# Kernel tuning notes

Measured on AMD Instinct MI355X. Metric: run time of the kernel, lower is better.

Reference implementation:

```python
import jax, jax.numpy as jnp
import numpy as np

N_NODES = 100000
N_EDGES = 1600000
IN_FEATS, N_HIDDEN, N_CLASSES = 128, 128, 32


def setup_inputs() -> dict:
    key = jax.random.key(0)
    ks = jax.random.split(key, 9)
    x = jax.random.normal(ks[0], (N_NODES, IN_FEATS), dtype=jnp.float32)
    src = jax.random.randint(ks[1], (N_EDGES,), 0, N_NODES, dtype=jnp.int64)
    dst = jax.random.randint(ks[2], (N_EDGES,), 0, N_NODES, dtype=jnp.int64)
    s1 = 1.0 / np.sqrt(IN_FEATS)
    s2 = 1.0 / np.sqrt(N_HIDDEN)
    W1 = jax.random.uniform(ks[3], (IN_FEATS, N_HIDDEN), jnp.float32, -s1, s1)
    b1 = jnp.zeros((N_HIDDEN,), jnp.float32)
    W2 = jax.random.uniform(ks[4], (N_HIDDEN, N_HIDDEN), jnp.float32, -s2, s2)
    b2 = jnp.zeros((N_HIDDEN,), jnp.float32)
    W3 = jax.random.uniform(ks[5], (N_HIDDEN, N_CLASSES), jnp.float32, -s2, s2)
    b3 = jnp.zeros((N_CLASSES,), jnp.float32)
    return {"x": x, "W1": W1, "b1": b1, "W2": W2, "b2": b2, "W3": W3, "b3": b3,
            "src": src, "dst": dst}


def _norms(src, dst):
    ones = jnp.ones((src.shape[0],), jnp.float32)
    deg_out = jax.ops.segment_sum(ones, src, num_segments=N_NODES)
    deg_in = jax.ops.segment_sum(ones, dst, num_segments=N_NODES)
    inv_sqrt = lambda d: jnp.where(d > 0, jax.lax.rsqrt(jnp.maximum(d, 1.0)), 0.0)
    return inv_sqrt(deg_out), inv_sqrt(deg_in)


def _sgconv(h, W, b, src, dst, norm_src, norm_dst):
    # D^-1/2 A D^-1/2 h, then linear
    m = h * norm_src[:, None]          # scale by source (out-degree) norm
    msg = m[src]                        # [E, F] gather
    agg = jax.ops.segment_sum(msg, dst, num_segments=N_NODES)  # scatter-add
    agg = agg * norm_dst[:, None]
    return agg @ W + b


def reference(x, W1, b1, W2, b2, W3, b3, src, dst):
    norm_src, norm_dst = _norms(src, dst)
    h = _sgconv(x, W1, b1, src, dst, norm_src, norm_dst)
    h = jax.nn.relu(h)
    h = _sgconv(h, W2, b2, src, dst, norm_src, norm_dst)
    h = jax.nn.relu(h)
    h = _sgconv(h, W3, b3, src, dst, norm_src, norm_dst)
    return h
```

## Files before the change

### kernel.cpp

```cpp
#include <hip/hip_runtime.h>


constexpr int FEAT = 128;
constexpr int STRIDE = 48;

typedef float f32x4 __attribute__((ext_vector_type(4)));
typedef short bf16x8 __attribute__((ext_vector_type(8)));

__device__ __forceinline__ unsigned short f2bf(float f) {
    unsigned int u = __builtin_bit_cast(unsigned int, f);
    unsigned int r = (u + 0x7FFFu + ((u >> 16) & 1u)) >> 16;
    return (unsigned short)r;
}
__device__ __forceinline__ float bf2f(unsigned short h) {
    unsigned int u = ((unsigned int)h) << 16;
    return __builtin_bit_cast(float, u);
}
__device__ __forceinline__ float bflo(unsigned int u) {
    return __builtin_bit_cast(float, u << 16);
}
__device__ __forceinline__ float bfhi(unsigned int u) {
    return __builtin_bit_cast(float, u & 0xffff0000u);
}
__device__ __forceinline__ unsigned int pack2(float a, float b) {
    return (unsigned int)f2bf(a) | ((unsigned int)f2bf(b) << 16);
}

__global__ __launch_bounds__(256) void degree_fill_kernel(const int* __restrict__ src,
                                                          const int* __restrict__ dst,
                                                          int* __restrict__ deg_out,
                                                          int* __restrict__ deg_in,
                                                          int* __restrict__ csr_pad, int E)
{
    int e = blockIdx.x * 256 + threadIdx.x;
    if (e < E) {
        int s = src[e];
        int d = dst[e];
        atomicAdd(&deg_out[s], 1);
        int pos = atomicAdd(&deg_in[d], 1);
        if (pos < STRIDE)
            csr_pad[(size_t)d * STRIDE + pos] = s;
    }
}

__global__ __launch_bounds__(256) void norm_kernel(const int* __restrict__ dout,
                                                   const int* __restrict__ din,
                                                   float* __restrict__ nsrc,
                                                   float* __restrict__ ndst, int N)
{
    int i = blockIdx.x * 256 + threadIdx.x;
    if (i < N) {
        int a = dout[i], b = din[i];
        nsrc[i] = (a > 0) ? rsqrtf((float)a) : 0.f;
        ndst[i] = (b > 0) ? rsqrtf((float)b) : 0.f;
    }
}

__global__ __launch_bounds__(256) void scale_bf16_kernel(const float* __restrict__ x,
                                                         const float* __restrict__ nsrc,
                                                         unsigned short* __restrict__ xb,
                                                         int ngroups)
{
    int i = blockIdx.x * 256 + threadIdx.x;
    if (i >= ngroups) return;
    int row = i >> 5;
    float ns = nsrc[row];
    float4 v = reinterpret_cast<const float4*>(x)[i];
    ushort4 o;
    o.x = f2bf(v.x * ns); o.y = f2bf(v.y * ns);
    o.z = f2bf(v.z * ns); o.w = f2bf(v.w * ns);
    reinterpret_cast<ushort4*>(xb)[i] = o;
}

__global__ __launch_bounds__(256) void gather128_kernel(const unsigned short* __restrict__ hb,
                                                        const float* __restrict__ ndst,
                                                        const int* __restrict__ deg_in,
                                                        const int* __restrict__ csr_pad,
                                                        unsigned short* __restrict__ aggb,
                                                        int N)
{
    const int node = blockIdx.x * 16 + (threadIdx.x >> 4);
    const int c = (threadIdx.x & 15) * 8;
    if (node >= N) return;
    const int* idx = csr_pad + (size_t)node * STRIDE;
    const int deg = min(deg_in[node], STRIDE);
    float4 a0 = make_float4(0.f, 0.f, 0.f, 0.f);
    float4 a1 = make_float4(0.f, 0.f, 0.f, 0.f);
    int j = 0;
    for (; j + 8 <= deg; j += 8) {
        int s[8];
        #pragma unroll
        for (int u = 0; u < 8; ++u) s[u] = idx[j + u];
        #pragma unroll
        for (int u = 0; u < 8; ++u) {
            uint4 v = *reinterpret_cast<const uint4*>(hb + (size_t)s[u] * 128 + c);
            a0.x += bflo(v.x); a0.y += bfhi(v.x);
            a0.z += bflo(v.y); a0.w += bfhi(v.y);
            a1.x += bflo(v.z); a1.y += bfhi(v.z);
            a1.z += bflo(v.w); a1.w += bfhi(v.w);
        }
    }
    for (; j < deg; ++j) {
        uint4 v = *reinterpret_cast<const uint4*>(hb + (size_t)idx[j] * 128 + c);
        a0.x += bflo(v.x); a0.y += bfhi(v.x);
        a0.z += bflo(v.y); a0.w += bfhi(v.y);
        a1.x += bflo(v.z); a1.y += bfhi(v.z);
        a1.z += bflo(v.w); a1.w += bfhi(v.w);
    }
    const float nd = ndst[node];
    uint4 o;
    o.x = pack2(a0.x * nd, a0.y * nd);
    o.y = pack2(a0.z * nd, a0.w * nd);
    o.z = pack2(a1.x * nd, a1.y * nd);
    o.w = pack2(a1.z * nd, a1.w * nd);
    *reinterpret_cast<uint4*>(aggb + (size_t)node * 128 + c) = o;
}

template<int NT, bool RELU, bool BIAS, bool SCALE>
__global__ __launch_bounds__(256) void mfma_gemm_kernel(
    const unsigned short* __restrict__ Ab,
    const float* __restrict__ W,
    const float* __restrict__ bias,
    const float* __restrict__ nsrc,
    unsigned short* __restrict__ Cb,
    int N)
{
    constexpr int NC = NT * 16;
    constexpr int SLD = (NC == 128) ? 136 : 32;
    __shared__ alignas(16) unsigned short Wl[NT * 4 * 64 * 8];
    __shared__ alignas(16) unsigned short Sc[4][16 * SLD];
    const int tid = threadIdx.x;

    for (int idx = tid; idx < NT * 4 * 64; idx += 256) {
        int l  = idx & 63;
        int k0 = (idx >> 6) & 3;
        int n0 = idx >> 8;
        int kb = k0 * 32 + (l >> 4) * 8;
        int n  = n0 * 16 + (l & 15);
        const float* wp = W + (size_t)kb * NC + n;
        unsigned int p0 = (unsigned int)f2bf(wp[0])      | ((unsigned int)f2bf(wp[NC])     << 16);
        unsigned int p1 = (unsigned int)f2bf(wp[2 * NC]) | ((unsigned int)f2bf(wp[3 * NC]) << 16);
        unsigned int p2 = (unsigned int)f2bf(wp[4 * NC]) | ((unsigned int)f2bf(wp[5 * NC]) << 16);
        unsigned int p3 = (unsigned int)f2bf(wp[6 * NC]) | ((unsigned int)f2bf(wp[7 * NC]) << 16);
        uint4 v = make_uint4(p0, p1, p2, p3);
        *reinterpret_cast<uint4*>(&Wl[idx * 8]) = v;
    }
    __syncthreads();

    const int wave = tid >> 6, lane = tid & 63;
    const int rowbase = blockIdx.x * 64 + wave * 16;
    const int arow = min(rowbase + (lane & 15), N - 1);
    const int koff = (lane >> 4) * 8;

    bf16x8 a[4];
    #pragma unroll
    for (int k0 = 0; k0 < 4; ++k0)
        a[k0] = *reinterpret_cast<const bf16x8*>(Ab + (size_t)arow * 128 + k0 * 32 + koff);

    f32x4 acc[NT];
    #pragma unroll
    for (int n0 = 0; n0 < NT; ++n0) acc[n0] = (f32x4)0.f;

    #pragma unroll
    for (int k0 = 0; k0 < 4; ++k0) {
        #pragma unroll
        for (int n0 = 0; n0 < NT; ++n0) {
            bf16x8 b = *reinterpret_cast<const bf16x8*>(&Wl[((n0 * 4 + k0) * 64 + lane) * 8]);
            acc[n0] = __builtin_amdgcn_mfma_f32_16x16x32_bf16(a[k0], b, acc[n0], 0, 0, 0);
        }
    }

    float rs[4];
    #pragma unroll
    for (int r = 0; r < 4; ++r) {
        int row = (lane >> 4) * 4 + r;
        rs[r] = SCALE ? nsrc[min(rowbase + row, N - 1)] : 1.f;
    }
    unsigned short* sc = &Sc[wave][0];
    #pragma unroll
    for (int n0 = 0; n0 < NT; ++n0) {
        int col = n0 * 16 + (lane & 15);
        float bv = BIAS ? bias[col] : 0.f;
        #pragma unroll
        for (int r = 0; r < 4; ++r) {
            int row = (lane >> 4) * 4 + r;
            float v = acc[n0][r] + bv;
            if (RELU) v = fmaxf(v, 0.f);
            v *= rs[r];
            sc[row * SLD + col] = f2bf(v);
        }
    }

    constexpr int CHUNKS = NC / 32;
    const int wrow = lane >> 2, q = lane & 3;
    const int grow = rowbase + wrow;
    if (grow < N) {
        #pragma unroll
        for (int t = 0; t < CHUNKS; ++t) {
            uint4 v = *reinterpret_cast<const uint4*>(&sc[wrow * SLD + q * (CHUNKS * 8) + t * 8]);
            *reinterpret_cast<uint4*>(Cb + (size_t)grow * NC + q * (CHUNKS * 8) + t * 8) = v;
        }
    }
}

__global__ __launch_bounds__(256) void gather32_kernel(const unsigned short* __restrict__ hb,
                                                       const float* __restrict__ ndst,
                                                       const int* __restrict__ deg_in,
                                                       const int* __restrict__ csr_pad,
                                                       const float* __restrict__ bias,
                                                       float* __restrict__ out, int N)
{
    const int node = blockIdx.x * 64 + (threadIdx.x >> 2);
    const int c = (threadIdx.x & 3) * 8;
    if (node >= N) return;
    const int* idx = csr_pad + (size_t)node * STRIDE;
    const int deg = min(deg_in[node], STRIDE);
    float4 a0 = make_float4(0.f, 0.f, 0.f, 0.f);
    float4 a1 = make_float4(0.f, 0.f, 0.f, 0.f);
    int j = 0;
    for (; j + 8 <= deg; j += 8) {
        int s[8];
        #pragma unroll
        for (int u = 0; u < 8; ++u) s[u] = idx[j + u];
        #pragma unroll
        for (int u = 0; u < 8; ++u) {
            uint4 v = *reinterpret_cast<const uint4*>(hb + (size_t)s[u] * 32 + c);
            a0.x += bflo(v.x); a0.y += bfhi(v.x);
            a0.z += bflo(v.y); a0.w += bfhi(v.y);
            a1.x += bflo(v.z); a1.y += bfhi(v.z);
            a1.z += bflo(v.w); a1.w += bfhi(v.w);
        }
    }
    for (; j < deg; ++j) {
        uint4 v = *reinterpret_cast<const uint4*>(hb + (size_t)idx[j] * 32 + c);
        a0.x += bflo(v.x); a0.y += bfhi(v.x);
        a0.z += bflo(v.y); a0.w += bfhi(v.y);
        a1.x += bflo(v.z); a1.y += bfhi(v.z);
        a1.z += bflo(v.w); a1.w += bfhi(v.w);
    }
    const float nd = ndst[node];
    float4 o0, o1;
    o0.x = a0.x * nd + bias[c + 0]; o0.y = a0.y * nd + bias[c + 1];
    o0.z = a0.z * nd + bias[c + 2]; o0.w = a0.w * nd + bias[c + 3];
    o1.x = a1.x * nd + bias[c + 4]; o1.y = a1.y * nd + bias[c + 5];
    o1.z = a1.z * nd + bias[c + 6]; o1.w = a1.w * nd + bias[c + 7];
    float* op = out + (size_t)node * 32 + c;
    *reinterpret_cast<float4*>(op)     = o0;
    *reinterpret_cast<float4*>(op + 4) = o1;
}

extern "C" void kernel_launch(void* const* d_in, const int* in_sizes, int n_in,
                              void* d_out, int out_size, void* d_ws, size_t ws_size,
                              hipStream_t stream)
{
    const float* x  = (const float*)d_in[0];
    const float* W1 = (const float*)d_in[1];
    const float* b1 = (const float*)d_in[2];
    const float* W2 = (const float*)d_in[3];
    const float* b2 = (const float*)d_in[4];
    const float* W3 = (const float*)d_in[5];
    const float* b3 = (const float*)d_in[6];
    const int*   src = (const int*)d_in[7];
    const int*   dst = (const int*)d_in[8];
    float* out = (float*)d_out;

    const int N = in_sizes[0] / FEAT;
    const int E = in_sizes[7];

    char* w = (char*)d_ws;
    float* norm_src  = (float*)w;                  w += (size_t)N * 4;
    float* norm_dst  = (float*)w;                  w += (size_t)N * 4;
    int*   deg_out   = (int*)w;                    w += (size_t)N * 4;
    int*   deg_in    = (int*)w;                    w += (size_t)N * 4;
    int*   csr_pad   = (int*)w;                    w += (size_t)N * STRIDE * 4;
    unsigned short* xb   = (unsigned short*)w;     w += (size_t)N * FEAT * 2;
    unsigned short* hb1  = (unsigned short*)w;     w += (size_t)N * FEAT * 2;
    unsigned short* aggb = (unsigned short*)w;
    unsigned short* h2b = xb;
    unsigned short* tb  = hb1;

    const int gblocks = (N + 63) / 64;

    hipMemsetAsync(deg_out, 0, 2 * (size_t)N * sizeof(int), stream);
    degree_fill_kernel<<<(E + 255) / 256, 256, 0, stream>>>(src, dst, deg_out, deg_in, csr_pad, E);
    norm_kernel<<<(N + 255) / 256, 256, 0, stream>>>(deg_out, deg_in, norm_src, norm_dst, N);

    scale_bf16_kernel<<<(N * 32 + 255) / 256, 256, 0, stream>>>(x, norm_src, xb, N * 32);

    gather128_kernel<<<(N + 15) / 16, 256, 0, stream>>>(
        xb, norm_dst, deg_in, csr_pad, aggb, N);
    mfma_gemm_kernel<8, true, true, true><<<gblocks, 256, 0, stream>>>(
        aggb, W1, b1, norm_src, hb1, N);

    gather128_kernel<<<(N + 15) / 16, 256, 0, stream>>>(
        hb1, norm_dst, deg_in, csr_pad, aggb, N);
    mfma_gemm_kernel<8, true, true, false><<<gblocks, 256, 0, stream>>>(
        aggb, W2, b2, nullptr, h2b, N);

    mfma_gemm_kernel<2, false, false, true><<<gblocks, 256, 0, stream>>>(
        h2b, W3, nullptr, norm_src, tb, N);
    gather32_kernel<<<(N + 63) / 64, 256, 0, stream>>>(
        tb, norm_dst, deg_in, csr_pad, b3, out, N);
}
```

Before: 386.6 us.

## Apply W1 before layer-1 aggregation and fuse with degree-fill kernel

Uses linearity to compute x@W1 first, inside the same launch as the degree/CSR build: extra blocks run an MFMA GEMM on raw x while the edge blocks do atomics. The layer-1 gather then applies the per-source norm on the fly, plus the destination norm, bias, ReLU and the next layer's source norm, all in one pass. This drops the separate scale kernel and the layer-1 GEMM launch, along with an intermediate bf16 round trip. In exchange the gather does an extra per-neighbour nsrc load, and the rounding order changes because bf16 is applied after the matmul rather than before aggregation.

```diff
diff --git a/kernel.cpp b/kernel.cpp
--- a/kernel.cpp
+++ b/kernel.cpp
@@ -1,7 +1,7 @@
 #include <hip/hip_runtime.h>
 
 
-constexpr int FEAT = 128;
+constexpr int FEAT   = 128;
 constexpr int STRIDE = 48;
 
 typedef float f32x4 __attribute__((ext_vector_type(4)));
@@ -12,10 +12,6 @@
     unsigned int r = (u + 0x7FFFu + ((u >> 16) & 1u)) >> 16;
     return (unsigned short)r;
 }
-__device__ __forceinline__ float bf2f(unsigned short h) {
-    unsigned int u = ((unsigned int)h) << 16;
-    return __builtin_bit_cast(float, u);
-}
 __device__ __forceinline__ float bflo(unsigned int u) {
     return __builtin_bit_cast(float, u << 16);
 }
@@ -26,20 +22,95 @@
     return (unsigned int)f2bf(a) | ((unsigned int)f2bf(b) << 16);
 }
 
-__global__ __launch_bounds__(256) void degree_fill_kernel(const int* __restrict__ src,
-                                                          const int* __restrict__ dst,
-                                                          int* __restrict__ deg_out,
-                                                          int* __restrict__ deg_in,
-                                                          int* __restrict__ csr_pad, int E)
-{
-    int e = blockIdx.x * 256 + threadIdx.x;
-    if (e < E) {
-        int s = src[e];
-        int d = dst[e];
-        atomicAdd(&deg_out[s], 1);
-        int pos = atomicAdd(&deg_in[d], 1);
-        if (pos < STRIDE)
-            csr_pad[(size_t)d * STRIDE + pos] = s;
+__global__ __launch_bounds__(256) void degree_fill_xw1_kernel(
+    const int* __restrict__ src, const int* __restrict__ dst,
+    const float* __restrict__ x, const float* __restrict__ W1,
+    int* __restrict__ deg_out, int* __restrict__ deg_in,
+    int* __restrict__ csr_pad, unsigned short* __restrict__ xw1,
+    int EB, int N, int E)
+{
+    __shared__ alignas(16) unsigned short Wl[8 * 4 * 64 * 8];
+    const int tid = threadIdx.x;
+
+    if ((int)blockIdx.x < EB) {
+        int e = (int)blockIdx.x * 256 + tid;
+        if (e < E) {
+            int s = src[e];
+            int d = dst[e];
+            atomicAdd(&deg_out[s], 1);
+            int pos = atomicAdd(&deg_in[d], 1);
+            if (pos < STRIDE)
+                csr_pad[(size_t)d * STRIDE + pos] = s;
+        }
+        return;
+    }
+
+    constexpr int NC = 128, SLD = 136;
+    const int gb = (int)blockIdx.x - EB;
+    for (int idx = tid; idx < 8 * 4 * 64; idx += 256) {
+        int l  = idx & 63;
+        int k0 = (idx >> 6) & 3;
+        int n0 = idx >> 8;
+        int kb = k0 * 32 + (l >> 4) * 8;
+        int n  = n0 * 16 + (l & 15);
+        const float* wp = W1 + (size_t)kb * NC + n;
+        uint4 v;
+        v.x = pack2(wp[0],      wp[NC]);
+        v.y = pack2(wp[2 * NC], wp[3 * NC]);
+        v.z = pack2(wp[4 * NC], wp[5 * NC]);
+        v.w = pack2(wp[6 * NC], wp[7 * NC]);
+        *reinterpret_cast<uint4*>(&Wl[idx * 8]) = v;
+    }
+    __syncthreads();
+
+    const int wave = tid >> 6, lane = tid & 63;
+    const int rowbase = gb * 64 + wave * 16;
+    const int arow = min(rowbase + (lane & 15), N - 1);
+    const int koff = (lane >> 4) * 8;
+
+    bf16x8 a[4];
+    #pragma unroll
+    for (int k0 = 0; k0 < 4; ++k0) {
+        const float* xp = x + (size_t)arow * 128 + k0 * 32 + koff;
+        float4 f0 = *reinterpret_cast<const float4*>(xp);
+        float4 f1 = *reinterpret_cast<const float4*>(xp + 4);
+        union { unsigned int u[4]; bf16x8 v; } r;
+        r.u[0] = pack2(f0.x, f0.y); r.u[1] = pack2(f0.z, f0.w);
+        r.u[2] = pack2(f1.x, f1.y); r.u[3] = pack2(f1.z, f1.w);
+        a[k0] = r.v;
+    }
+
+    f32x4 acc[8];
+    #pragma unroll
+    for (int n0 = 0; n0 < 8; ++n0) acc[n0] = (f32x4)0.f;
+    #pragma unroll
+    for (int k0 = 0; k0 < 4; ++k0) {
+        #pragma unroll
+        for (int n0 = 0; n0 < 8; ++n0) {
+            bf16x8 b = *reinterpret_cast<const bf16x8*>(&Wl[((n0 * 4 + k0) * 64 + lane) * 8]);
+            acc[n0] = __builtin_amdgcn_mfma_f32_16x16x32_bf16(a[k0], b, acc[n0], 0, 0, 0);
+        }
+    }
+
+    __syncthreads();
+    unsigned short* sc = &Wl[wave * 16 * SLD];
+    #pragma unroll
+    for (int n0 = 0; n0 < 8; ++n0) {
+        int col = n0 * 16 + (lane & 15);
+        #pragma unroll
+        for (int r = 0; r < 4; ++r) {
+            int row = (lane >> 4) * 4 + r;
+            sc[row * SLD + col] = f2bf(acc[n0][r]);
+        }
+    }
+    const int wrow = lane >> 2, q = lane & 3;
+    const int grow = rowbase + wrow;
+    if (grow < N) {
+        #pragma unroll
+        for (int t = 0; t < 4; ++t) {
+            uint4 v = *reinterpret_cast<const uint4*>(&sc[wrow * SLD + q * 32 + t * 8]);
+            *reinterpret_cast<uint4*>(xw1 + (size_t)grow * 128 + q * 32 + t * 8) = v;
+        }
     }
 }
 
@@ -56,28 +127,14 @@
     }
 }
 
-__global__ __launch_bounds__(256) void scale_bf16_kernel(const float* __restrict__ x,
-                                                         const float* __restrict__ nsrc,
-                                                         unsigned short* __restrict__ xb,
-                                                         int ngroups)
-{
-    int i = blockIdx.x * 256 + threadIdx.x;
-    if (i >= ngroups) return;
-    int row = i >> 5;
-    float ns = nsrc[row];
-    float4 v = reinterpret_cast<const float4*>(x)[i];
-    ushort4 o;
-    o.x = f2bf(v.x * ns); o.y = f2bf(v.y * ns);
-    o.z = f2bf(v.z * ns); o.w = f2bf(v.w * ns);
-    reinterpret_cast<ushort4*>(xb)[i] = o;
-}
-
-__global__ __launch_bounds__(256) void gather128_kernel(const unsigned short* __restrict__ hb,
-                                                        const float* __restrict__ ndst,
-                                                        const int* __restrict__ deg_in,
-                                                        const int* __restrict__ csr_pad,
-                                                        unsigned short* __restrict__ aggb,
-                                                        int N)
+__global__ __launch_bounds__(256) void gather1_kernel(const unsigned short* __restrict__ xw1,
+                                                      const float* __restrict__ nsrc,
+                                                      const float* __restrict__ ndst,
+                                                      const int* __restrict__ deg_in,
+                                                      const int* __restrict__ csr_pad,
+                                                      const float* __restrict__ b1,
+                                                      unsigned short* __restrict__ hb1,
+                                                      int N)
 {
     const int node = blockIdx.x * 16 + (threadIdx.x >> 4);
     const int c = (threadIdx.x & 15) * 8;
@@ -89,6 +146,71 @@
     int j = 0;
     for (; j + 8 <= deg; j += 8) {
         int s[8];
+        float ns[8];
+        #pragma unroll
+        for (int u = 0; u < 8; ++u) s[u] = idx[j + u];
+        #pragma unroll
+        for (int u = 0; u < 8; ++u) ns[u] = nsrc[s[u]];
+        #pragma unroll
+        for (int u = 0; u < 8; ++u) {
+            uint4 v = *reinterpret_cast<const uint4*>(xw1 + (size_t)s[u] * 128 + c);
+            a0.x = fmaf(bflo(v.x), ns[u], a0.x);
+            a0.y = fmaf(bfhi(v.x), ns[u], a0.y);
+            a0.z = fmaf(bflo(v.y), ns[u], a0.z);
+            a0.w = fmaf(bfhi(v.y), ns[u], a0.w);
+            a1.x = fmaf(bflo(v.z), ns[u], a1.x);
+            a1.y = fmaf(bfhi(v.z), ns[u], a1.y);
+            a1.z = fmaf(bflo(v.w), ns[u], a1.z);
+            a1.w = fmaf(bfhi(v.w), ns[u], a1.w);
+        }
+    }
+    for (; j < deg; ++j) {
+        int s0 = idx[j];
+        float n0 = nsrc[s0];
+        uint4 v = *reinterpret_cast<const uint4*>(xw1 + (size_t)s0 * 128 + c);
+        a0.x = fmaf(bflo(v.x), n0, a0.x);
+        a0.y = fmaf(bfhi(v.x), n0, a0.y);
+        a0.z = fmaf(bflo(v.y), n0, a0.z);
+        a0.w = fmaf(bfhi(v.y), n0, a0.w);
+        a1.x = fmaf(bflo(v.z), n0, a1.x);
+        a1.y = fmaf(bfhi(v.z), n0, a1.y);
+        a1.z = fmaf(bflo(v.w), n0, a1.z);
+        a1.w = fmaf(bfhi(v.w), n0, a1.w);
+    }
+    const float nd = ndst[node];
+    const float nsn = nsrc[node];
+    const float* bp = b1 + c;
+    float v0 = fmaxf(a0.x * nd + bp[0], 0.f) * nsn;
+    float v1 = fmaxf(a0.y * nd + bp[1], 0.f) * nsn;
+    float v2 = fmaxf(a0.z * nd + bp[2], 0.f) * nsn;
+    float v3 = fmaxf(a0.w * nd + bp[3], 0.f) * nsn;
+    float v4 = fmaxf(a1.x * nd + bp[4], 0.f) * nsn;
+    float v5 = fmaxf(a1.y * nd + bp[5], 0.f) * nsn;
+    float v6 = fmaxf(a1.z * nd + bp[6], 0.f) * nsn;
+    float v7 = fmaxf(a1.w * nd + bp[7], 0.f) * nsn;
+    uint4 o;
+    o.x = pack2(v0, v1); o.y = pack2(v2, v3);
+    o.z = pack2(v4, v5); o.w = pack2(v6, v7);
+    *reinterpret_cast<uint4*>(hb1 + (size_t)node * 128 + c) = o;
+}
+
+__global__ __launch_bounds__(256) void gather128_kernel(const unsigned short* __restrict__ hb,
+                                                        const float* __restrict__ ndst,
+                                                        const int* __restrict__ deg_in,
+                                                        const int* __restrict__ csr_pad,
+                                                        unsigned short* __restrict__ aggb,
+                                                        int N)
+{
+    const int node = blockIdx.x * 16 + (threadIdx.x >> 4);
+    const int c = (threadIdx.x & 15) * 8;
+    if (node >= N) return;
+    const int* idx = csr_pad + (size_t)node * STRIDE;
+    const int deg = min(deg_in[node], STRIDE);
+    float4 a0 = make_float4(0.f, 0.f, 0.f, 0.f);
+    float4 a1 = make_float4(0.f, 0.f, 0.f, 0.f);
+    int j = 0;
+    for (; j + 8 <= deg; j += 8) {
+        int s[8];
         #pragma unroll
         for (int u = 0; u < 8; ++u) s[u] = idx[j + u];
         #pragma unroll
@@ -138,11 +260,11 @@
         int kb = k0 * 32 + (l >> 4) * 8;
         int n  = n0 * 16 + (l & 15);
         const float* wp = W + (size_t)kb * NC + n;
-        unsigned int p0 = (unsigned int)f2bf(wp[0])      | ((unsigned int)f2bf(wp[NC])     << 16);
-        unsigned int p1 = (unsigned int)f2bf(wp[2 * NC]) | ((unsigned int)f2bf(wp[3 * NC]) << 16);
-        unsigned int p2 = (unsigned int)f2bf(wp[4 * NC]) | ((unsigned int)f2bf(wp[5 * NC]) << 16);
-        unsigned int p3 = (unsigned int)f2bf(wp[6 * NC]) | ((unsigned int)f2bf(wp[7 * NC]) << 16);
-        uint4 v = make_uint4(p0, p1, p2, p3);
+        uint4 v;
+        v.x = pack2(wp[0],      wp[NC]);
+        v.y = pack2(wp[2 * NC], wp[3 * NC]);
+        v.z = pack2(wp[4 * NC], wp[5 * NC]);
+        v.w = pack2(wp[6 * NC], wp[7 * NC]);
         *reinterpret_cast<uint4*>(&Wl[idx * 8]) = v;
     }
     __syncthreads();
@@ -266,6 +388,8 @@
 
     const int N = in_sizes[0] / FEAT;
     const int E = in_sizes[7];
+    const int EB = (E + 255) / 256;
+    const int GB = (N + 63) / 64;
 
     char* w = (char*)d_ws;
     float* norm_src  = (float*)w;                  w += (size_t)N * 4;
@@ -273,24 +397,21 @@
     int*   deg_out   = (int*)w;                    w += (size_t)N * 4;
     int*   deg_in    = (int*)w;                    w += (size_t)N * 4;
     int*   csr_pad   = (int*)w;                    w += (size_t)N * STRIDE * 4;
-    unsigned short* xb   = (unsigned short*)w;     w += (size_t)N * FEAT * 2;
+    unsigned short* xw1  = (unsigned short*)w;     w += (size_t)N * FEAT * 2;
     unsigned short* hb1  = (unsigned short*)w;     w += (size_t)N * FEAT * 2;
     unsigned short* aggb = (unsigned short*)w;
-    unsigned short* h2b = xb;
+    unsigned short* h2b = xw1;
     unsigned short* tb  = hb1;
 
     const int gblocks = (N + 63) / 64;
 
     hipMemsetAsync(deg_out, 0, 2 * (size_t)N * sizeof(int), stream);
-    degree_fill_kernel<<<(E + 255) / 256, 256, 0, stream>>>(src, dst, deg_out, deg_in, csr_pad, E);
+    degree_fill_xw1_kernel<<<EB + GB, 256, 0, stream>>>(
+        src, dst, x, W1, deg_out, deg_in, csr_pad, xw1, EB, N, E);
     norm_kernel<<<(N + 255) / 256, 256, 0, stream>>>(deg_out, deg_in, norm_src, norm_dst, N);
 
-    scale_bf16_kernel<<<(N * 32 + 255) / 256, 256, 0, stream>>>(x, norm_src, xb, N * 32);
-
-    gather128_kernel<<<(N + 15) / 16, 256, 0, stream>>>(
-        xb, norm_dst, deg_in, csr_pad, aggb, N);
-    mfma_gemm_kernel<8, true, true, true><<<gblocks, 256, 0, stream>>>(
-        aggb, W1, b1, norm_src, hb1, N);
+    gather1_kernel<<<(N + 15) / 16, 256, 0, stream>>>(
+        xw1, norm_src, norm_dst, deg_in, csr_pad, b1, hb1, N);
 
     gather128_kernel<<<(N + 15) / 16, 256, 0, stream>>>(
         hb1, norm_dst, deg_in, csr_pad, aggb, N);
```

New measurement: 393.7 us. About the same (+1.8%).
